# Optimization experiments

Measured on AMD Instinct MI355X. Metric: run time of the kernel, lower is better.

Reference implementation:

```python
import jax, jax.numpy as jnp
import numpy as np

B, S, D_IN, D_OUT, H = 4, 2048, 1024, 1024, 16
DH = D_OUT // H


def setup_inputs() -> dict:
    key = jax.random.key(0)
    k1, k2, k3 = jax.random.split(key, 3)
    payload = jax.random.normal(k1, (B, S, D_IN), dtype=jnp.float32)
    w_qkv = jax.random.normal(k2, (D_IN, 3 * D_OUT), dtype=jnp.float32) * (D_IN ** -0.5)
    w_out = jax.random.normal(k3, (D_OUT, D_OUT), dtype=jnp.float32) * (D_OUT ** -0.5)
    b_out = jnp.zeros((D_OUT,), dtype=jnp.float32)
    return {"payload": payload, "w_qkv": w_qkv, "w_out": w_out, "b_out": b_out}


def reference(payload, w_qkv, w_out, b_out):
    b, t, _ = payload.shape
    h, dh = H, DH
    qkv = payload @ w_qkv  # [b, t, 3*D_OUT]
    q, k, v = jnp.split(qkv, 3, axis=-1)
    # [b, t, h, dh] -> [b, h, t, dh]
    q = q.reshape(b, t, h, dh).transpose(0, 2, 1, 3)
    k = k.reshape(b, t, h, dh).transpose(0, 2, 1, 3)
    v = v.reshape(b, t, h, dh).transpose(0, 2, 1, 3)
    scores = jnp.einsum("bhqd,bhkd->bhqk", q, k) / jnp.sqrt(jnp.float32(dh))
    causal = jnp.tril(jnp.ones((t, t), dtype=bool))  # True = keep
    scores = jnp.where(causal, scores, -jnp.inf)
    weights = jax.nn.softmax(scores, axis=-1)
    # dropout_rate = 0.0 -> identity
    ctx = jnp.einsum("bhqk,bhkd->bhqd", weights, v)
    ctx = ctx.transpose(0, 2, 1, 3).reshape(b, t, h * dh)
    return ctx @ w_out + b_out
```

## Files before the change

kernel.cpp:

```cpp
#include <hip/hip_runtime.h>

#define NB 4
#define NS 2048
#define NH 16
#define NDH 64

typedef short bf16x8 __attribute__((ext_vector_type(8)));
typedef short bf16x4 __attribute__((ext_vector_type(4)));
typedef float f32x4 __attribute__((ext_vector_type(4)));
typedef unsigned short u16;
typedef unsigned int u32;

static __device__ __forceinline__ u16 f2bf(float f) {
  unsigned u = __float_as_uint(f);
  u += 0x7fffu + ((u >> 16) & 1u);
  return (u16)(u >> 16);
}

#define GLDS(gp, lp) __builtin_amdgcn_global_load_lds( \
    (const __attribute__((address_space(1))) void*)(gp), \
    (__attribute__((address_space(3))) void*)(lp), 16, 0, 0)

__global__ void cvt_k(const float* __restrict__ in, u16* __restrict__ out, int n) {
  int i = (blockIdx.x * 256 + threadIdx.x) * 8;
  if (i >= n) return;
  float4 a = *(const float4*)&in[i];
  float4 b = *(const float4*)&in[i + 4];
  bf16x8 u;
  u[0] = (short)f2bf(a.x); u[1] = (short)f2bf(a.y);
  u[2] = (short)f2bf(a.z); u[3] = (short)f2bf(a.w);
  u[4] = (short)f2bf(b.x); u[5] = (short)f2bf(b.y);
  u[6] = (short)f2bf(b.z); u[7] = (short)f2bf(b.w);
  *(bf16x8*)&out[i] = u;
}

__global__ void trcvt_k(const float* __restrict__ in, u16* __restrict__ out, int R, int C) {
  __shared__ float t[32][33];
  int c0 = blockIdx.x * 32, r0 = blockIdx.y * 32;
  int tx = threadIdx.x & 7, ty = threadIdx.x >> 3;
  float4 v = *(const float4*)&in[(size_t)(r0 + ty) * C + c0 + tx * 4];
  t[ty][tx * 4 + 0] = v.x; t[ty][tx * 4 + 1] = v.y;
  t[ty][tx * 4 + 2] = v.z; t[ty][tx * 4 + 3] = v.w;
  __syncthreads();
  ushort4 o;
  o.x = f2bf(t[tx * 4 + 0][ty]); o.y = f2bf(t[tx * 4 + 1][ty]);
  o.z = f2bf(t[tx * 4 + 2][ty]); o.w = f2bf(t[tx * 4 + 3][ty]);
  *(ushort4*)&out[(size_t)(c0 + ty) * R + r0 + tx * 4] = o;
}

template<int MODE, int WM>
__global__ __launch_bounds__(WM * 128)
void gemm_k(const u16* __restrict__ A, const u16* __restrict__ Bt,
            int M, int N, int K,
            u16* __restrict__ Qo, u16* __restrict__ Ko, u16* __restrict__ VTo,
            float* __restrict__ Co, const float* __restrict__ bias) {
  constexpr int T  = WM * 128;
  constexpr int BM = WM * 64;
  constexpr int RA = 4;
  constexpr int RB = 1024 / T;
  __shared__ __align__(16) u16 As[BM * 64];
  __shared__ __align__(16) u16 Bs[128 * 64];
  const int tid = threadIdx.x;
  const int w = tid >> 6, l = tid & 63;
  const int lr = l & 15, lg = l >> 4;
  const int wr = w >> 1, wc = w & 1;
  const int m0 = blockIdx.y * BM, n0 = blockIdx.x * 128;
  const int swz = (lr & 7) << 4;

  f32x4 acc[4][4] = {};

  const int nk = K >> 6;
  for (int kt = 0; kt < nk; ++kt) {
    __syncthreads();
    const int k0 = kt * 64;
#pragma unroll
    for (int r2 = 0; r2 < RA; ++r2) {
      int c = r2 * T + tid;
      int row = c >> 3;
      int scolb = ((c & 7) * 16) ^ ((row & 7) << 4);
      GLDS(A + (size_t)(m0 + row) * K + k0 + (scolb >> 1),
           (char*)As + (size_t)r2 * T * 16 + w * 1024);
    }
#pragma unroll
    for (int r2 = 0; r2 < RB; ++r2) {
      int c = r2 * T + tid;
      int row = c >> 3;
      int scolb = ((c & 7) * 16) ^ ((row & 7) << 4);
      GLDS(Bt + (size_t)(n0 + row) * K + k0 + (scolb >> 1),
           (char*)Bs + (size_t)r2 * T * 16 + w * 1024);
    }
    __syncthreads();

#pragma unroll
    for (int kk = 0; kk < 2; ++kk) {
      bf16x8 af[4];
#pragma unroll
      for (int mi = 0; mi < 4; ++mi)
        af[mi] = *(const bf16x8*)((const char*)As +
                  ((wr * 64 + mi * 16 + lr) * 128 + ((kk * 64 + lg * 16) ^ swz)));
#pragma unroll
      for (int ni = 0; ni < 4; ++ni) {
        bf16x8 bfr = *(const bf16x8*)((const char*)Bs +
                  ((wc * 64 + ni * 16 + lr) * 128 + ((kk * 64 + lg * 16) ^ swz)));
#pragma unroll
        for (int mi = 0; mi < 4; ++mi)
          acc[mi][ni] = __builtin_amdgcn_mfma_f32_16x16x32_bf16(af[mi], bfr, acc[mi][ni], 0, 0, 0);
      }
    }
  }

#pragma unroll
  for (int mi = 0; mi < 4; ++mi) {
#pragma unroll
    for (int ni = 0; ni < 4; ++ni) {
#pragma unroll
      for (int r = 0; r < 4; ++r) {
        int gm = m0 + wr * 64 + mi * 16 + lg * 4 + r;
        int gn = n0 + wc * 64 + ni * 16 + lr;
        float v = acc[mi][ni][r];
        if (MODE == 0) {
          int which = gn >> 10, hd = gn & 1023;
          int b = gm >> 11, s = gm & 2047;
          int bh = b * NH + (hd >> 6), dh = hd & 63;
          if (which == 0)      Qo[((size_t)bh * NS + s) * NDH + dh] = f2bf(v * 0.1803368801111204f);
          else if (which == 1) Ko[((size_t)bh * NS + s) * NDH + dh] = f2bf(v);
          else                 VTo[((size_t)bh * NDH + dh) * NS + s] = f2bf(v);
        } else {
          Co[(size_t)gm * N + gn] = v + bias[gn];
        }
      }
    }
  }
}

__global__ __launch_bounds__(512)
void attn_k(const u16* __restrict__ Q, const u16* __restrict__ Kg,
            const u16* __restrict__ VTg, u16* __restrict__ CTX) {
  const int bh = blockIdx.x;
  const int pr = blockIdx.y;
  const int tid = threadIdx.x, w = tid >> 6, l = tid & 63;
  const int lr = l & 15, lg = l >> 4;
  const u16* Qh  = Q   + (size_t)bh * NS * NDH;
  const u16* Kh  = Kg  + (size_t)bh * NS * NDH;
  const u16* Vth = VTg + (size_t)bh * NDH * NS;

  __shared__ __align__(16) u16 Ks[2][64 * 64];
  __shared__ __align__(16) u16 Vs[2][64 * 64];

  const int srow_ = tid >> 3;
  const int colb  = (tid & 7) * 16;
  const int scolb = colb ^ ((srow_ & 7) << 4);
  const int kSrcOff = srow_ * NDH + (scolb >> 1);
  const int vSrcOff = srow_ * NS + (scolb >> 1);
  const int ldsOff  = w * 1024;

#define STAGE(t, buf) do {                                          \
    GLDS(Kh  + (size_t)(t) * 64 * NDH + kSrcOff, (char*)Ks[buf] + ldsOff); \
    GLDS(Vth + (size_t)(t) * 64       + vSrcOff, (char*)Vs[buf] + ldsOff); \
  } while (0)

  const int swz = (lr & 7) << 4;
  const int b = bh >> 4, h = bh & 15;

  for (int pass = 0; pass < 2; ++pass) {
    const int qt = pass == 0 ? pr : 15 - pr;

    const int qrow = qt * 128 + w * 16 + lr;
    bf16x8 qf[2];
    qf[0] = *(const bf16x8*)&Qh[(size_t)qrow * NDH + 0 * 32 + lg * 8];
    qf[1] = *(const bf16x8*)&Qh[(size_t)qrow * NDH + 1 * 32 + lg * 8];

    f32x4 o[4] = {};
    float lrun = 0.f;
    const int qmin = qt * 128 + w * 16;

    __syncthreads();
    STAGE(0, 0);
    __syncthreads();

    const int NT = 2 * qt + 2;
    for (int kt = 0; kt < NT; ++kt) {
      const int cur = kt & 1;
      if (kt + 1 < NT) STAGE(kt + 1, cur ^ 1);

      f32x4 sc[4] = {};
#pragma unroll
      for (int kk = 0; kk < 2; ++kk) {
#pragma unroll
        for (int kg = 0; kg < 4; ++kg) {
          bf16x8 kf = *(const bf16x8*)((const char*)Ks[cur] +
                       ((kg * 16 + lr) * 128 + ((kk * 64 + lg * 16) ^ swz)));
          sc[kg] = __builtin_amdgcn_mfma_f32_16x16x32_bf16(kf, qf[kk], sc[kg], 0, 0, 0);
        }
      }

      float sum = 0.f;
      if (kt * 64 + 63 > qmin) {
#pragma unroll
        for (int kg = 0; kg < 4; ++kg)
#pragma unroll
          for (int r = 0; r < 4; ++r) {
            int kglob = kt * 64 + kg * 16 + lg * 4 + r;
            float e = (kglob > qrow) ? 0.f : exp2f(sc[kg][r]);
            sc[kg][r] = e; sum += e;
          }
      } else {
#pragma unroll
        for (int kg = 0; kg < 4; ++kg)
#pragma unroll
          for (int r = 0; r < 4; ++r) {
            float e = exp2f(sc[kg][r]);
            sc[kg][r] = e; sum += e;
          }
      }
      lrun += sum;

#pragma unroll
      for (int half = 0; half < 2; ++half) {
        union { u32 wd[4]; bf16x8 v; } pk;
#pragma unroll
        for (int w2 = 0; w2 < 4; ++w2) {
          float lo = sc[half * 2 + (w2 >> 1)][2 * (w2 & 1)];
          float hi = sc[half * 2 + (w2 >> 1)][2 * (w2 & 1) + 1];
          asm("v_cvt_pk_bf16_f32 %0, %1, %2" : "=v"(pk.wd[w2]) : "v"(lo), "v"(hi));
        }
        bf16x8 pf = pk.v;
#pragma unroll
        for (int dhg = 0; dhg < 4; ++dhg) {
          const char* vrow = (const char*)Vs[cur] + (dhg * 16 + lr) * 128;
          bf16x4 va = *(const bf16x4*)(vrow + ((half * 64 + lg * 8) ^ swz));
          bf16x4 vb = *(const bf16x4*)(vrow + ((half * 64 + 32 + lg * 8) ^ swz));
          bf16x8 vf = __builtin_shufflevector(va, vb, 0, 1, 2, 3, 4, 5, 6, 7);
          o[dhg] = __builtin_amdgcn_mfma_f32_16x16x32_bf16(pf, vf, o[dhg], 0, 0, 0);
        }
      }

      __syncthreads();
    }

    lrun += __shfl_xor(lrun, 16);
    lrun += __shfl_xor(lrun, 32);
    float linv = 1.0f / lrun;
#pragma unroll
    for (int r = 0; r < 4; ++r) {
      float lq = __shfl(linv, (l & 48) | (lg * 4 + r));
      int srow = qt * 128 + w * 16 + lg * 4 + r;
      size_t base = ((size_t)(b * NS + srow)) * (NH * NDH) + h * NDH;
#pragma unroll
      for (int dhg = 0; dhg < 4; ++dhg)
        CTX[base + dhg * 16 + lr] = f2bf(o[dhg][r] * lq);
    }
  }
#undef STAGE
}

extern "C" void kernel_launch(void* const* d_in, const int* in_sizes, int n_in,
                              void* d_out, int out_size, void* d_ws, size_t ws_size,
                              hipStream_t stream) {
  const float* payload = (const float*)d_in[0];
  const float* w_qkv   = (const float*)d_in[1];
  const float* w_out   = (const float*)d_in[2];
  const float* b_out   = (const float*)d_in[3];
  float* out = (float*)d_out;

  char* ws = (char*)d_ws;
  size_t o0 = 0;
  u16* Xb    = (u16*)(ws + o0); o0 += (size_t)8192 * 1024 * 2;
  u16* Wqkvt = (u16*)(ws + o0); o0 += (size_t)3072 * 1024 * 2;
  u16* Woutt = (u16*)(ws + o0); o0 += (size_t)1024 * 1024 * 2;
  u16* Qb    = (u16*)(ws + o0); o0 += (size_t)64 * 2048 * 64 * 2;
  u16* Kb    = (u16*)(ws + o0); o0 += (size_t)64 * 2048 * 64 * 2;
  u16* VTb   = (u16*)(ws + o0); o0 += (size_t)64 * 64 * 2048 * 2;
  u16* CTX   = Xb;

  cvt_k<<<dim3(4096), dim3(256), 0, stream>>>(payload, Xb, 8192 * 1024);
  trcvt_k<<<dim3(96, 32), dim3(256), 0, stream>>>(w_qkv, Wqkvt, 1024, 3072);
  trcvt_k<<<dim3(32, 32), dim3(256), 0, stream>>>(w_out, Woutt, 1024, 1024);
  gemm_k<0, 4><<<dim3(24, 32), dim3(512), 0, stream>>>(Xb, Wqkvt, 8192, 3072, 1024,
                                                       Qb, Kb, VTb, nullptr, nullptr);
  attn_k<<<dim3(64, 8), dim3(512), 0, stream>>>(Qb, Kb, VTb, CTX);
  gemm_k<1, 2><<<dim3(8, 64), dim3(256), 0, stream>>>(CTX, Woutt, 8192, 1024, 1024,
                                                      nullptr, nullptr, nullptr, out, b_out);
}
```

Baseline: 198.5 us.

## Add triple-buffered, interleaved-prefetch QKV GEMM kernel with priority-boosted MFMA phases

Replaces the QKV projection GEMM with a dedicated kernel that keeps three LDS stages and prefetches two k-tiles ahead via global_load_lds. The prefetch is split into chunks interleaved between four MFMA phases, separated by barriers and with s_setprio raised around the MFMA blocks, to overlap global-to-LDS traffic with matrix math. The output-projection GEMM loses its MODE template and keeps only the fp32 bias epilogue. The added barriers and manual vmcnt waits bring sync overhead and scheduling fragility, and the three stages use more LDS per block.

```diff
diff --git a/kernel.cpp b/kernel.cpp
--- a/kernel.cpp
+++ b/kernel.cpp
@@ -48,11 +48,144 @@
   *(ushort4*)&out[(size_t)(c0 + ty) * R + r0 + tx * 4] = o;
 }
 
-template<int MODE, int WM>
+#define BAR   do { __builtin_amdgcn_s_barrier(); __builtin_amdgcn_sched_barrier(0); } while (0)
+#define VMC(n) do { asm volatile("s_waitcnt vmcnt(" #n ")" ::: "memory"); \
+                    __builtin_amdgcn_sched_barrier(0); } while (0)
+
+__global__ __launch_bounds__(512)
+void gemm8_k(const u16* __restrict__ A, const u16* __restrict__ Bt,
+             u16* __restrict__ Qo, u16* __restrict__ Ko, u16* __restrict__ VTo) {
+  constexpr int Kd = 1024, NK = 16;
+  __shared__ __align__(16) u16 As[3][256 * 64];
+  __shared__ __align__(16) u16 Bs[3][128 * 64];
+  const int tid = threadIdx.x, w = tid >> 6, l = tid & 63;
+  const int lr = l & 15, lg = l >> 4;
+  const int wr = w >> 1, wc = w & 1;
+  const int m0 = blockIdx.y * 256, n0 = blockIdx.x * 128;
+  const int swz = (lr & 7) << 4;
+
+  int aSrc[4], bSrc[2], dOff[4];
+#pragma unroll
+  for (int r2 = 0; r2 < 4; ++r2) {
+    int c = r2 * 512 + tid;
+    int row = c >> 3;
+    int sb = ((c & 7) * 16) ^ ((row & 7) << 4);
+    aSrc[r2] = row * Kd + (sb >> 1);
+    if (r2 < 2) bSrc[r2] = row * Kd + (sb >> 1);
+    dOff[r2] = r2 * 8192 + w * 1024;
+  }
+
+#define STG_A(t, r2) GLDS(A  + (size_t)m0 * Kd + (t) * 64 + aSrc[r2], (char*)As[(t) % 3] + dOff[r2])
+#define STG_B(t, r2) GLDS(Bt + (size_t)n0 * Kd + (t) * 64 + bSrc[r2], (char*)Bs[(t) % 3] + dOff[r2])
+#define RD_A(mi, kk) (*(const bf16x8*)((const char*)As[cur] + \
+    ((wr * 64 + (mi) * 16 + lr) * 128 + (((kk) * 64 + lg * 16) ^ swz))))
+#define RD_B(ni, kk) (*(const bf16x8*)((const char*)Bs[cur] + \
+    ((wc * 64 + (ni) * 16 + lr) * 128 + (((kk) * 64 + lg * 16) ^ swz))))
+
+  f32x4 acc[4][4] = {};
+
+  STG_A(0, 0); STG_A(0, 1); STG_A(0, 2); STG_A(0, 3); STG_B(0, 0); STG_B(0, 1);
+  STG_A(1, 0); STG_A(1, 1); STG_A(1, 2); STG_A(1, 3); STG_B(1, 0); STG_B(1, 1);
+  VMC(6);
+  BAR;
+
+  for (int t = 0; t < NK; ++t) {
+    const int cur = t % 3;
+    const bool pf = (t + 2 < NK);
+    bf16x8 af0, af1, af2, af3, b0, b1, b2, b3;
+
+    af0 = RD_A(0, 0); af1 = RD_A(1, 0); af2 = RD_A(2, 0); af3 = RD_A(3, 0);
+    b0 = RD_B(0, 0); b1 = RD_B(1, 0);
+    if (pf) { STG_A(t + 2, 0); STG_A(t + 2, 1); }
+    BAR;
+    __builtin_amdgcn_s_setprio(1);
+    acc[0][0] = __builtin_amdgcn_mfma_f32_16x16x32_bf16(af0, b0, acc[0][0], 0, 0, 0);
+    acc[1][0] = __builtin_amdgcn_mfma_f32_16x16x32_bf16(af1, b0, acc[1][0], 0, 0, 0);
+    acc[2][0] = __builtin_amdgcn_mfma_f32_16x16x32_bf16(af2, b0, acc[2][0], 0, 0, 0);
+    acc[3][0] = __builtin_amdgcn_mfma_f32_16x16x32_bf16(af3, b0, acc[3][0], 0, 0, 0);
+    acc[0][1] = __builtin_amdgcn_mfma_f32_16x16x32_bf16(af0, b1, acc[0][1], 0, 0, 0);
+    acc[1][1] = __builtin_amdgcn_mfma_f32_16x16x32_bf16(af1, b1, acc[1][1], 0, 0, 0);
+    acc[2][1] = __builtin_amdgcn_mfma_f32_16x16x32_bf16(af2, b1, acc[2][1], 0, 0, 0);
+    acc[3][1] = __builtin_amdgcn_mfma_f32_16x16x32_bf16(af3, b1, acc[3][1], 0, 0, 0);
+    __builtin_amdgcn_s_setprio(0);
+    BAR;
+
+    b2 = RD_B(2, 0); b3 = RD_B(3, 0);
+    if (pf) { STG_A(t + 2, 2); STG_A(t + 2, 3); }
+    BAR;
+    __builtin_amdgcn_s_setprio(1);
+    acc[0][2] = __builtin_amdgcn_mfma_f32_16x16x32_bf16(af0, b2, acc[0][2], 0, 0, 0);
+    acc[1][2] = __builtin_amdgcn_mfma_f32_16x16x32_bf16(af1, b2, acc[1][2], 0, 0, 0);
+    acc[2][2] = __builtin_amdgcn_mfma_f32_16x16x32_bf16(af2, b2, acc[2][2], 0, 0, 0);
+    acc[3][2] = __builtin_amdgcn_mfma_f32_16x16x32_bf16(af3, b2, acc[3][2], 0, 0, 0);
+    acc[0][3] = __builtin_amdgcn_mfma_f32_16x16x32_bf16(af0, b3, acc[0][3], 0, 0, 0);
+    acc[1][3] = __builtin_amdgcn_mfma_f32_16x16x32_bf16(af1, b3, acc[1][3], 0, 0, 0);
+    acc[2][3] = __builtin_amdgcn_mfma_f32_16x16x32_bf16(af2, b3, acc[2][3], 0, 0, 0);
+    acc[3][3] = __builtin_amdgcn_mfma_f32_16x16x32_bf16(af3, b3, acc[3][3], 0, 0, 0);
+    __builtin_amdgcn_s_setprio(0);
+    BAR;
+
+    af0 = RD_A(0, 1); af1 = RD_A(1, 1); af2 = RD_A(2, 1); af3 = RD_A(3, 1);
+    b0 = RD_B(0, 1); b1 = RD_B(1, 1);
+    if (pf) STG_B(t + 2, 0);
+    BAR;
+    __builtin_amdgcn_s_setprio(1);
+    acc[0][0] = __builtin_amdgcn_mfma_f32_16x16x32_bf16(af0, b0, acc[0][0], 0, 0, 0);
+    acc[1][0] = __builtin_amdgcn_mfma_f32_16x16x32_bf16(af1, b0, acc[1][0], 0, 0, 0);
+    acc[2][0] = __builtin_amdgcn_mfma_f32_16x16x32_bf16(af2, b0, acc[2][0], 0, 0, 0);
+    acc[3][0] = __builtin_amdgcn_mfma_f32_16x16x32_bf16(af3, b0, acc[3][0], 0, 0, 0);
+    acc[0][1] = __builtin_amdgcn_mfma_f32_16x16x32_bf16(af0, b1, acc[0][1], 0, 0, 0);
+    acc[1][1] = __builtin_amdgcn_mfma_f32_16x16x32_bf16(af1, b1, acc[1][1], 0, 0, 0);
+    acc[2][1] = __builtin_amdgcn_mfma_f32_16x16x32_bf16(af2, b1, acc[2][1], 0, 0, 0);
+    acc[3][1] = __builtin_amdgcn_mfma_f32_16x16x32_bf16(af3, b1, acc[3][1], 0, 0, 0);
+    __builtin_amdgcn_s_setprio(0);
+    BAR;
+
+    b2 = RD_B(2, 1); b3 = RD_B(3, 1);
+    if (pf) STG_B(t + 2, 1);
+    BAR;
+    __builtin_amdgcn_s_setprio(1);
+    acc[0][2] = __builtin_amdgcn_mfma_f32_16x16x32_bf16(af0, b2, acc[0][2], 0, 0, 0);
+    acc[1][2] = __builtin_amdgcn_mfma_f32_16x16x32_bf16(af1, b2, acc[1][2], 0, 0, 0);
+    acc[2][2] = __builtin_amdgcn_mfma_f32_16x16x32_bf16(af2, b2, acc[2][2], 0, 0, 0);
+    acc[3][2] = __builtin_amdgcn_mfma_f32_16x16x32_bf16(af3, b2, acc[3][2], 0, 0, 0);
+    acc[0][3] = __builtin_amdgcn_mfma_f32_16x16x32_bf16(af0, b3, acc[0][3], 0, 0, 0);
+    acc[1][3] = __builtin_amdgcn_mfma_f32_16x16x32_bf16(af1, b3, acc[1][3], 0, 0, 0);
+    acc[2][3] = __builtin_amdgcn_mfma_f32_16x16x32_bf16(af2, b3, acc[2][3], 0, 0, 0);
+    acc[3][3] = __builtin_amdgcn_mfma_f32_16x16x32_bf16(af3, b3, acc[3][3], 0, 0, 0);
+    __builtin_amdgcn_s_setprio(0);
+    if (t + 2 < NK) { VMC(6); } else { VMC(0); }
+    BAR;
+  }
+
+#pragma unroll
+  for (int mi = 0; mi < 4; ++mi) {
+#pragma unroll
+    for (int ni = 0; ni < 4; ++ni) {
+#pragma unroll
+      for (int r = 0; r < 4; ++r) {
+        int gm = m0 + wr * 64 + mi * 16 + lg * 4 + r;
+        int gn = n0 + wc * 64 + ni * 16 + lr;
+        float v = acc[mi][ni][r];
+        int which = gn >> 10, hd = gn & 1023;
+        int b = gm >> 11, s = gm & 2047;
+        int bh = b * NH + (hd >> 6), dh = hd & 63;
+        if (which == 0)      Qo[((size_t)bh * NS + s) * NDH + dh] = f2bf(v * 0.1803368801111204f);
+        else if (which == 1) Ko[((size_t)bh * NS + s) * NDH + dh] = f2bf(v);
+        else                 VTo[((size_t)bh * NDH + dh) * NS + s] = f2bf(v);
+      }
+    }
+  }
+#undef STG_A
+#undef STG_B
+#undef RD_A
+#undef RD_B
+}
+
+template<int WM>
 __global__ __launch_bounds__(WM * 128)
 void gemm_k(const u16* __restrict__ A, const u16* __restrict__ Bt,
             int M, int N, int K,
-            u16* __restrict__ Qo, u16* __restrict__ Ko, u16* __restrict__ VTo,
             float* __restrict__ Co, const float* __restrict__ bias) {
   constexpr int T  = WM * 128;
   constexpr int BM = WM * 64;
@@ -110,27 +243,15 @@
   }
 
 #pragma unroll
-  for (int mi = 0; mi < 4; ++mi) {
-#pragma unroll
-    for (int ni = 0; ni < 4; ++ni) {
+  for (int mi = 0; mi < 4; ++mi)
+#pragma unroll
+    for (int ni = 0; ni < 4; ++ni)
 #pragma unroll
       for (int r = 0; r < 4; ++r) {
         int gm = m0 + wr * 64 + mi * 16 + lg * 4 + r;
         int gn = n0 + wc * 64 + ni * 16 + lr;
-        float v = acc[mi][ni][r];
-        if (MODE == 0) {
-          int which = gn >> 10, hd = gn & 1023;
-          int b = gm >> 11, s = gm & 2047;
-          int bh = b * NH + (hd >> 6), dh = hd & 63;
-          if (which == 0)      Qo[((size_t)bh * NS + s) * NDH + dh] = f2bf(v * 0.1803368801111204f);
-          else if (which == 1) Ko[((size_t)bh * NS + s) * NDH + dh] = f2bf(v);
-          else                 VTo[((size_t)bh * NDH + dh) * NS + s] = f2bf(v);
-        } else {
-          Co[(size_t)gm * N + gn] = v + bias[gn];
-        }
-      }
-    }
-  }
+        Co[(size_t)gm * N + gn] = acc[mi][ni][r] + bias[gn];
+      }
 }
 
 __global__ __launch_bounds__(512)
@@ -276,9 +397,8 @@
   cvt_k<<<dim3(4096), dim3(256), 0, stream>>>(payload, Xb, 8192 * 1024);
   trcvt_k<<<dim3(96, 32), dim3(256), 0, stream>>>(w_qkv, Wqkvt, 1024, 3072);
   trcvt_k<<<dim3(32, 32), dim3(256), 0, stream>>>(w_out, Woutt, 1024, 1024);
-  gemm_k<0, 4><<<dim3(24, 32), dim3(512), 0, stream>>>(Xb, Wqkvt, 8192, 3072, 1024,
-                                                       Qb, Kb, VTb, nullptr, nullptr);
+  gemm8_k<<<dim3(24, 32), dim3(512), 0, stream>>>(Xb, Wqkvt, Qb, Kb, VTb);
   attn_k<<<dim3(64, 8), dim3(512), 0, stream>>>(Qb, Kb, VTb, CTX);
-  gemm_k<1, 2><<<dim3(8, 64), dim3(256), 0, stream>>>(CTX, Woutt, 8192, 1024, 1024,
-                                                      nullptr, nullptr, nullptr, out, b_out);
-}
+  gemm_k<2><<<dim3(8, 64), dim3(256), 0, stream>>>(CTX, Woutt, 8192, 1024, 1024,
+                                                   out, b_out);
+}
```

Measured after the change: 220.1 us. 1.11x slower.
